# Kernel optimization log

Hardware: AMD Instinct MI355X
Metric: run time of the kernel (lower is better)

## Reference

```python
import jax, jax.numpy as jnp
import numpy as np

N_IN = 100_000
N_OUT = 400_000
K = 27          # 3^3 kernel offsets
C_IN = 64
C_OUT = 32


def setup_inputs() -> dict:
    key = jax.random.key(0)
    k1, k2, k3, k4 = jax.random.split(key, 4)
    feats = jax.random.normal(k1, (N_IN, C_IN), dtype=jnp.float32)
    # Minkowski-style weight: one [C_in, C_out] matrix per kernel offset
    weight = jax.random.normal(k2, (K, C_IN, C_OUT), dtype=jnp.float32) * (1.0 / np.sqrt(C_IN))
    # kernel maps: for each offset, M=N_IN (in_idx, out_idx) pairs
    in_map = jax.random.randint(k3, (K, N_IN), 0, N_IN, dtype=jnp.int64)
    out_map = jax.random.randint(k4, (K, N_IN), 0, N_OUT, dtype=jnp.int64)
    return {"feats": feats, "weight": weight, "in_map": in_map,
            "out_map": out_map, "n_out": N_OUT}


def reference(feats, weight, in_map, out_map, n_out):
    # gather-GEMM-scatter, vectorized over the K kernel offsets
    gathered = feats[in_map]                          # [K, M, C_in]
    msgs = jnp.einsum('kmc,kcd->kmd', gathered, weight)  # [K, M, C_out]
    out = jnp.zeros((n_out, msgs.shape[-1]), dtype=feats.dtype)
    out = out.at[out_map.reshape(-1)].add(msgs.reshape(-1, msgs.shape[-1]))
    return out
```

## Files before the change

kernel.cpp:

```cpp
#include <hip/hip_runtime.h>
#include <hip/hip_bf16.h>
#include <hip/hip_fp16.h>


using short8  = __attribute__((ext_vector_type(8))) short;
using floatx4 = __attribute__((ext_vector_type(4))) float;
using f32x4   = __attribute__((ext_vector_type(4))) float;
using i32x4   = __attribute__((ext_vector_type(4))) int;

constexpr int KOFF = 27;
constexpr int NIN  = 100000;
constexpr int NOUT = 400000;
constexpr int CIN  = 64;
constexpr int COUT = 32;
constexpr int MSGS = NIN;
constexpr int TILES = MSGS / 16;
constexpr int WPB   = 4;
constexpr int BLK_PER_K = 128;
constexpr int WSTRIDE = BLK_PER_K * WPB;

constexpr size_t ACC_BYTES   = (size_t)NOUT * COUT * 2;
constexpr size_t FEATS_BYTES = (size_t)NIN * CIN * 2;

constexpr int CVT_BLOCKS  = (NIN * CIN / 8) / 256;
constexpr int ZERO_BLOCKS = (int)(ACC_BYTES / 16) / 256;

__device__ __forceinline__ short f2bf(float f) {
    union { float f; unsigned u; } v; v.f = f;
    unsigned r = v.u + 0x7fff + ((v.u >> 16) & 1u);
    return (short)(r >> 16);
}

__global__ __launch_bounds__(256) void prep_kernel(
    const float* __restrict__ f, ushort* __restrict__ b, f32x4* __restrict__ accz)
{
    if (blockIdx.x < CVT_BLOCKS) {
        const int t = blockIdx.x * 256 + threadIdx.x;
        const f32x4* p = (const f32x4*)(f + (size_t)t * 8);
        f32x4 lo = __builtin_nontemporal_load(p);
        f32x4 hi = __builtin_nontemporal_load(p + 1);
        short8 v;
        v[0]=f2bf(lo[0]); v[1]=f2bf(lo[1]); v[2]=f2bf(lo[2]); v[3]=f2bf(lo[3]);
        v[4]=f2bf(hi[0]); v[5]=f2bf(hi[1]); v[6]=f2bf(hi[2]); v[7]=f2bf(hi[3]);
        *(short8*)(b + (size_t)t * 8) = v;
    } else {
        const int t = (blockIdx.x - CVT_BLOCKS) * 256 + threadIdx.x;
        f32x4 z = {0.f, 0.f, 0.f, 0.f};
        __builtin_nontemporal_store(z, accz + t);
    }
}

__global__ __launch_bounds__(256) void spconv_pipe_kernel(
    const ushort* __restrict__ feats_bf,
    const float*  __restrict__ weight,
    const int*    __restrict__ in_map,
    const int*    __restrict__ out_map,
    __half2*      __restrict__ accum)
{
    const int k    = blockIdx.y;
    const int wave = threadIdx.x >> 6;
    const int lane = threadIdx.x & 63;
    const int col  = lane & 15;
    const int quad = lane >> 4;
    const int kM   = k * MSGS;

    const float* Wk = weight + k * (CIN * COUT);
    short8 bfr[2][2];
    #pragma unroll
    for (int s = 0; s < 2; ++s)
        #pragma unroll
        for (int t = 0; t < 2; ++t)
            #pragma unroll
            for (int j = 0; j < 8; ++j)
                bfr[s][t][j] = f2bf(Wk[(s * 32 + quad * 8 + j) * COUT + 2 * col + t]);

    auto load_maps = [&](int t, int& inr, i32x4& orow) {
        const int tt = (t < TILES) ? t : (TILES - 1);
        const int mb = kM + tt * 16;
        inr  = __builtin_nontemporal_load(in_map + mb + col);
        orow = __builtin_nontemporal_load((const i32x4*)(out_map + mb + quad * 4));
    };
    auto load_feats = [&](int inr, short8& a0, short8& a1) {
        const ushort* ar = feats_bf + inr * CIN;
        a0 = *(const short8*)(ar + quad * 8);
        a1 = *(const short8*)(ar + 32 + quad * 8);
    };

    const int t0 = blockIdx.x * WPB + wave;

    int inrA; i32x4 orowA; load_maps(t0,               inrA, orowA);
    int inrB; i32x4 orowB; load_maps(t0 +     WSTRIDE, inrB, orowB);
    int inrC; i32x4 orowC; load_maps(t0 + 2 * WSTRIDE, inrC, orowC);
    short8 a0A, a1A; load_feats(inrA, a0A, a1A);
    short8 a0B, a1B; load_feats(inrB, a0B, a1B);

    for (int t = t0; t < TILES; t += WSTRIDE) {
        int inrD; i32x4 orowD;
        load_maps(t + 3 * WSTRIDE, inrD, orowD);
        short8 a0C, a1C;
        load_feats(inrC, a0C, a1C);

        floatx4 acc0 = {0.f, 0.f, 0.f, 0.f};
        floatx4 acc1 = {0.f, 0.f, 0.f, 0.f};
        acc0 = __builtin_amdgcn_mfma_f32_16x16x32_bf16(a0A, bfr[0][0], acc0, 0, 0, 0);
        acc1 = __builtin_amdgcn_mfma_f32_16x16x32_bf16(a0A, bfr[0][1], acc1, 0, 0, 0);
        acc0 = __builtin_amdgcn_mfma_f32_16x16x32_bf16(a1A, bfr[1][0], acc0, 0, 0, 0);
        acc1 = __builtin_amdgcn_mfma_f32_16x16x32_bf16(a1A, bfr[1][1], acc1, 0, 0, 0);

        const int orr[4] = {orowA[0], orowA[1], orowA[2], orowA[3]};
        #pragma unroll
        for (int i = 0; i < 4; ++i) {
            __half2 h = __floats2half2_rn(acc0[i], acc1[i]);
            unsafeAtomicAdd(accum + orr[i] * 16 + col, h);
        }

        inrA = inrB; a0A = a0B; a1A = a1B; orowA = orowB;
        inrB = inrC; a0B = a0C; a1B = a1C; orowB = orowC;
        inrC = inrD; orowC = orowD;
    }
}

__global__ __launch_bounds__(256) void spconv_fp16acc_f32feats_kernel(
    const float*  __restrict__ feats_f32,
    const float*  __restrict__ weight,
    const int*    __restrict__ in_map,
    const int*    __restrict__ out_map,
    __half2*      __restrict__ accum)
{
    const int k    = blockIdx.y;
    const int wave = threadIdx.x >> 6;
    const int lane = threadIdx.x & 63;
    const int col  = lane & 15;
    const int quad = lane >> 4;
    const int tile = blockIdx.x * WPB + wave;
    if (tile >= TILES) return;
    const int m0 = tile * 16;
    const long long mapbase = (long long)k * MSGS;

    const int in_row = in_map[mapbase + m0 + col];
    int orow[4];
    #pragma unroll
    for (int i = 0; i < 4; ++i) orow[i] = out_map[mapbase + m0 + quad * 4 + i];

    const float* Wk = weight + k * (CIN * COUT);
    short8 bfr[2][2];
    #pragma unroll
    for (int s = 0; s < 2; ++s)
        #pragma unroll
        for (int t = 0; t < 2; ++t)
            #pragma unroll
            for (int j = 0; j < 8; ++j)
                bfr[s][t][j] = f2bf(Wk[(s * 32 + quad * 8 + j) * COUT + 2 * col + t]);

    const float* ar = feats_f32 + (long long)in_row * CIN + quad * 8;
    const float4* p0 = (const float4*)ar;
    const float4* p1 = (const float4*)(ar + 32);
    float4 l0 = p0[0], h0 = p0[1], l1 = p1[0], h1 = p1[1];
    short8 a0, a1;
    a0[0]=f2bf(l0.x); a0[1]=f2bf(l0.y); a0[2]=f2bf(l0.z); a0[3]=f2bf(l0.w);
    a0[4]=f2bf(h0.x); a0[5]=f2bf(h0.y); a0[6]=f2bf(h0.z); a0[7]=f2bf(h0.w);
    a1[0]=f2bf(l1.x); a1[1]=f2bf(l1.y); a1[2]=f2bf(l1.z); a1[3]=f2bf(l1.w);
    a1[4]=f2bf(h1.x); a1[5]=f2bf(h1.y); a1[6]=f2bf(h1.z); a1[7]=f2bf(h1.w);

    floatx4 acc0 = {0.f, 0.f, 0.f, 0.f};
    floatx4 acc1 = {0.f, 0.f, 0.f, 0.f};
    acc0 = __builtin_amdgcn_mfma_f32_16x16x32_bf16(a0, bfr[0][0], acc0, 0, 0, 0);
    acc1 = __builtin_amdgcn_mfma_f32_16x16x32_bf16(a0, bfr[0][1], acc1, 0, 0, 0);
    acc0 = __builtin_amdgcn_mfma_f32_16x16x32_bf16(a1, bfr[1][0], acc0, 0, 0, 0);
    acc1 = __builtin_amdgcn_mfma_f32_16x16x32_bf16(a1, bfr[1][1], acc1, 0, 0, 0);

    #pragma unroll
    for (int i = 0; i < 4; ++i) {
        __half2 h = __floats2half2_rn(acc0[i], acc1[i]);
        unsafeAtomicAdd(accum + (long long)orow[i] * 16 + col, h);
    }
}

__global__ __launch_bounds__(256) void spconv_f32atomic_kernel(
    const float* __restrict__ feats,
    const float* __restrict__ weight,
    const int*   __restrict__ in_map,
    const int*   __restrict__ out_map,
    float*       __restrict__ out)
{
    const int k    = blockIdx.y;
    const int wave = threadIdx.x >> 6;
    const int lane = threadIdx.x & 63;
    const int col  = lane & 15;
    const int quad = lane >> 4;
    const int tile = blockIdx.x * WPB + wave;
    if (tile >= TILES) return;
    const int m0 = tile * 16;
    const long long mapbase = (long long)k * MSGS;

    const float* Wk = weight + k * (CIN * COUT);
    short8 bfr[2][2];
    #pragma unroll
    for (int s = 0; s < 2; ++s)
        #pragma unroll
        for (int t = 0; t < 2; ++t)
            #pragma unroll
            for (int j = 0; j < 8; ++j)
                bfr[s][t][j] = f2bf(Wk[(s * 32 + quad * 8 + j) * COUT + t * 16 + col]);

    const int in_row = in_map[mapbase + m0 + col];
    const float* arow = feats + (long long)in_row * CIN + quad * 8;

    floatx4 acc0 = {0.f, 0.f, 0.f, 0.f};
    floatx4 acc1 = {0.f, 0.f, 0.f, 0.f};
    #pragma unroll
    for (int s = 0; s < 2; ++s) {
        const float4* p = (const float4*)(arow + s * 32);
        float4 lo = p[0], hi = p[1];
        short8 a;
        a[0]=f2bf(lo.x); a[1]=f2bf(lo.y); a[2]=f2bf(lo.z); a[3]=f2bf(lo.w);
        a[4]=f2bf(hi.x); a[5]=f2bf(hi.y); a[6]=f2bf(hi.z); a[7]=f2bf(hi.w);
        acc0 = __builtin_amdgcn_mfma_f32_16x16x32_bf16(a, bfr[s][0], acc0, 0, 0, 0);
        acc1 = __builtin_amdgcn_mfma_f32_16x16x32_bf16(a, bfr[s][1], acc1, 0, 0, 0);
    }
    #pragma unroll
    for (int i = 0; i < 4; ++i) {
        const int orow = out_map[mapbase + m0 + quad * 4 + i];
        float* po = out + (long long)orow * COUT;
        atomicAdd(po + col,      acc0[i]);
        atomicAdd(po + col + 16, acc1[i]);
    }
}

__global__ __launch_bounds__(256) void h2_to_f32_kernel(
    const __half2* __restrict__ acc, float* __restrict__ out)
{
    const int t = blockIdx.x * blockDim.x + threadIdx.x;
    const __half2* p = acc + (size_t)t * 4;
    float2 f0 = __half22float2(p[0]);
    float2 f1 = __half22float2(p[1]);
    float2 f2 = __half22float2(p[2]);
    float2 f3 = __half22float2(p[3]);
    f32x4* o = (f32x4*)out + (size_t)t * 2;
    f32x4 o0 = {f0.x, f0.y, f1.x, f1.y};
    f32x4 o1 = {f2.x, f2.y, f3.x, f3.y};
    __builtin_nontemporal_store(o0, o);
    __builtin_nontemporal_store(o1, o + 1);
}

extern "C" void kernel_launch(void* const* d_in, const int* in_sizes, int n_in,
                              void* d_out, int out_size, void* d_ws, size_t ws_size,
                              hipStream_t stream) {
    const float* feats   = (const float*)d_in[0];
    const float* weight  = (const float*)d_in[1];
    const int*   in_map  = (const int*)d_in[2];
    const int*   out_map = (const int*)d_in[3];
    float*       out     = (float*)d_out;

    if (ws_size >= ACC_BYTES + FEATS_BYTES) {
        __half2* accum    = (__half2*)d_ws;
        ushort*  feats_bf = (ushort*)((char*)d_ws + ACC_BYTES);

        prep_kernel<<<CVT_BLOCKS + ZERO_BLOCKS, 256, 0, stream>>>(
            feats, feats_bf, (f32x4*)accum);
        spconv_pipe_kernel<<<dim3(BLK_PER_K, KOFF), 256, 0, stream>>>(
            feats_bf, weight, in_map, out_map, accum);
        h2_to_f32_kernel<<<(NOUT * 16 / 4) / 256, 256, 0, stream>>>(accum, out);
    } else if (ws_size >= ACC_BYTES) {
        __half2* accum = (__half2*)d_ws;
        hipMemsetAsync(accum, 0, ACC_BYTES, stream);
        spconv_fp16acc_f32feats_kernel<<<dim3((TILES + WPB - 1) / WPB, KOFF), 256, 0, stream>>>(
            feats, weight, in_map, out_map, accum);
        h2_to_f32_kernel<<<(NOUT * 16 / 4) / 256, 256, 0, stream>>>(accum, out);
    } else {
        hipMemsetAsync(d_out, 0, (size_t)out_size * sizeof(float), stream);
        spconv_f32atomic_kernel<<<dim3((TILES + WPB - 1) / WPB, KOFF), 256, 0, stream>>>(
            feats, weight, in_map, out_map, out);
    }
}
```

Baseline: 253.8 us.

## Fuse prep, gather-GEMM-scatter and convert into one cooperative kernel

Replaces the three-kernel sequence (bf16 convert plus accumulator zeroing, MFMA gather-GEMM-scatter with fp16 atomics, fp16-to-fp32 conversion) with one persistent cooperative kernel that uses grid-wide syncs between phases. The aim is to remove kernel launch gaps and tail idle time between stages. The cost is two grid barriers and a smaller fixed grid (75 blocks per offset instead of 128), which changes how the work is spread and may lower memory parallelism. If the cooperative launch fails, it falls back to the old three-kernel path.

```diff
diff --git a/kernel.cpp b/kernel.cpp
--- a/kernel.cpp
+++ b/kernel.cpp
@@ -1,7 +1,10 @@
 #include <hip/hip_runtime.h>
 #include <hip/hip_bf16.h>
 #include <hip/hip_fp16.h>
-
+#include <hip/hip_cooperative_groups.h>
+
+
+namespace cg = cooperative_groups;
 
 using short8  = __attribute__((ext_vector_type(8))) short;
 using floatx4 = __attribute__((ext_vector_type(4))) float;
@@ -16,6 +19,12 @@
 constexpr int MSGS = NIN;
 constexpr int TILES = MSGS / 16;
 constexpr int WPB   = 4;
+
+constexpr int CBLK_PER_K = 75;
+constexpr int COOP_BLOCKS = CBLK_PER_K * KOFF;
+constexpr int CWSTRIDE = CBLK_PER_K * WPB;
+constexpr int CTHREADS = COOP_BLOCKS * 256;
+
 constexpr int BLK_PER_K = 128;
 constexpr int WSTRIDE = BLK_PER_K * WPB;
 
@@ -30,6 +39,116 @@
     unsigned r = v.u + 0x7fff + ((v.u >> 16) & 1u);
     return (short)(r >> 16);
 }
+
+__global__ __launch_bounds__(256, 8) void spconv_fused_kernel(
+    const float* __restrict__ feats_f32,
+    ushort*      __restrict__ feats_bf,
+    const float* __restrict__ weight,
+    const int*   __restrict__ in_map,
+    const int*   __restrict__ out_map,
+    __half2*     __restrict__ accum,
+    float*       __restrict__ out)
+{
+    cg::grid_group grid = cg::this_grid();
+    const int gtid = blockIdx.x * 256 + threadIdx.x;
+
+    for (int t = gtid; t < NIN * CIN / 8; t += CTHREADS) {
+        const f32x4* p = (const f32x4*)(feats_f32 + (size_t)t * 8);
+        f32x4 lo = __builtin_nontemporal_load(p);
+        f32x4 hi = __builtin_nontemporal_load(p + 1);
+        short8 v;
+        v[0]=f2bf(lo[0]); v[1]=f2bf(lo[1]); v[2]=f2bf(lo[2]); v[3]=f2bf(lo[3]);
+        v[4]=f2bf(hi[0]); v[5]=f2bf(hi[1]); v[6]=f2bf(hi[2]); v[7]=f2bf(hi[3]);
+        *(short8*)(feats_bf + (size_t)t * 8) = v;
+    }
+    {
+        f32x4* accz = (f32x4*)accum;
+        f32x4 z = {0.f, 0.f, 0.f, 0.f};
+        for (int t = gtid; t < (int)(ACC_BYTES / 16); t += CTHREADS)
+            __builtin_nontemporal_store(z, accz + t);
+    }
+    grid.sync();
+
+    {
+        const int k    = blockIdx.x / CBLK_PER_K;
+        const int bx   = blockIdx.x % CBLK_PER_K;
+        const int wave = threadIdx.x >> 6;
+        const int lane = threadIdx.x & 63;
+        const int col  = lane & 15;
+        const int quad = lane >> 4;
+        const int kM   = k * MSGS;
+
+        const float* Wk = weight + k * (CIN * COUT);
+        short8 bfr[2][2];
+        #pragma unroll
+        for (int s = 0; s < 2; ++s)
+            #pragma unroll
+            for (int t = 0; t < 2; ++t)
+                #pragma unroll
+                for (int j = 0; j < 8; ++j)
+                    bfr[s][t][j] = f2bf(Wk[(s * 32 + quad * 8 + j) * COUT + 2 * col + t]);
+
+        auto load_maps = [&](int t, int& inr, i32x4& orow) {
+            const int tt = (t < TILES) ? t : (TILES - 1);
+            const int mb = kM + tt * 16;
+            inr  = __builtin_nontemporal_load(in_map + mb + col);
+            orow = __builtin_nontemporal_load((const i32x4*)(out_map + mb + quad * 4));
+        };
+        auto load_feats = [&](int inr, short8& a0, short8& a1) {
+            const ushort* ar = feats_bf + inr * CIN;
+            a0 = *(const short8*)(ar + quad * 8);
+            a1 = *(const short8*)(ar + 32 + quad * 8);
+        };
+
+        const int t0 = bx * WPB + wave;
+
+        int inrA; i32x4 orowA; load_maps(t0,                inrA, orowA);
+        int inrB; i32x4 orowB; load_maps(t0 +     CWSTRIDE, inrB, orowB);
+        int inrC; i32x4 orowC; load_maps(t0 + 2 * CWSTRIDE, inrC, orowC);
+        short8 a0A, a1A; load_feats(inrA, a0A, a1A);
+        short8 a0B, a1B; load_feats(inrB, a0B, a1B);
+
+        for (int t = t0; t < TILES; t += CWSTRIDE) {
+            int inrD; i32x4 orowD;
+            load_maps(t + 3 * CWSTRIDE, inrD, orowD);
+            short8 a0C, a1C;
+            load_feats(inrC, a0C, a1C);
+
+            floatx4 acc0 = {0.f, 0.f, 0.f, 0.f};
+            floatx4 acc1 = {0.f, 0.f, 0.f, 0.f};
+            acc0 = __builtin_amdgcn_mfma_f32_16x16x32_bf16(a0A, bfr[0][0], acc0, 0, 0, 0);
+            acc1 = __builtin_amdgcn_mfma_f32_16x16x32_bf16(a0A, bfr[0][1], acc1, 0, 0, 0);
+            acc0 = __builtin_amdgcn_mfma_f32_16x16x32_bf16(a1A, bfr[1][0], acc0, 0, 0, 0);
+            acc1 = __builtin_amdgcn_mfma_f32_16x16x32_bf16(a1A, bfr[1][1], acc1, 0, 0, 0);
+
+            const int orr[4] = {orowA[0], orowA[1], orowA[2], orowA[3]};
+            #pragma unroll
+            for (int i = 0; i < 4; ++i) {
+                __half2 h = __floats2half2_rn(acc0[i], acc1[i]);
+                unsafeAtomicAdd(accum + orr[i] * 16 + col, h);
+            }
+
+            inrA = inrB; a0A = a0B; a1A = a1B; orowA = orowB;
+            inrB = inrC; a0B = a0C; a1B = a1C; orowB = orowC;
+            inrC = inrD; orowC = orowD;
+        }
+    }
+    grid.sync();
+
+    for (int t = gtid; t < NOUT * 16 / 4; t += CTHREADS) {
+        const __half2* p = accum + (size_t)t * 4;
+        float2 f0 = __half22float2(p[0]);
+        float2 f1 = __half22float2(p[1]);
+        float2 f2 = __half22float2(p[2]);
+        float2 f3 = __half22float2(p[3]);
+        f32x4* o = (f32x4*)out + (size_t)t * 2;
+        f32x4 o0 = {f0.x, f0.y, f1.x, f1.y};
+        f32x4 o1 = {f2.x, f2.y, f3.x, f3.y};
+        __builtin_nontemporal_store(o0, o);
+        __builtin_nontemporal_store(o1, o + 1);
+    }
+}
+
 
 __global__ __launch_bounds__(256) void prep_kernel(
     const float* __restrict__ f, ushort* __restrict__ b, f32x4* __restrict__ accz)
@@ -256,11 +375,19 @@
         __half2* accum    = (__half2*)d_ws;
         ushort*  feats_bf = (ushort*)((char*)d_ws + ACC_BYTES);
 
-        prep_kernel<<<CVT_BLOCKS + ZERO_BLOCKS, 256, 0, stream>>>(
-            feats, feats_bf, (f32x4*)accum);
-        spconv_pipe_kernel<<<dim3(BLK_PER_K, KOFF), 256, 0, stream>>>(
-            feats_bf, weight, in_map, out_map, accum);
-        h2_to_f32_kernel<<<(NOUT * 16 / 4) / 256, 256, 0, stream>>>(accum, out);
+        void* args[] = {(void*)&feats, (void*)&feats_bf, (void*)&weight,
+                        (void*)&in_map, (void*)&out_map, (void*)&accum,
+                        (void*)&out};
+        hipError_t e = hipLaunchCooperativeKernel(
+            (const void*)spconv_fused_kernel, dim3(COOP_BLOCKS), dim3(256),
+            args, 0, stream);
+        if (e != hipSuccess) {
+            prep_kernel<<<CVT_BLOCKS + ZERO_BLOCKS, 256, 0, stream>>>(
+                feats, feats_bf, (f32x4*)accum);
+            spconv_pipe_kernel<<<dim3(BLK_PER_K, KOFF), 256, 0, stream>>>(
+                feats_bf, weight, in_map, out_map, accum);
+            h2_to_f32_kernel<<<(NOUT * 16 / 4) / 256, 256, 0, stream>>>(accum, out);
+        }
     } else if (ws_size >= ACC_BYTES) {
         __half2* accum = (__half2*)d_ws;
         hipMemsetAsync(accum, 0, ACC_BYTES, stream);
```

After: 752.3 us. 2.96x slower.

## Drop bf16 feature pre-conversion; gather fp32 rows and convert in pipelined loop

Applied to the files above, without the earlier changes.

Removes the prep kernel that converted the features to bf16 and zeroed the accumulator, replacing it with hipMemsetAsync for zeroing. The pipelined main kernel now gathers fp32 feature rows directly, keeping raw fp32 registers for upcoming tiles and converting them to bf16 one stage before use. This avoids writing and re-reading a bf16 copy of the features, but doubles the bytes per gathered row and adds conversion ALU work plus register pressure inside the loop. The pipeline depth for feature data changes, and the code leaves the tile A row index stale, though it is no longer needed.

```diff
diff --git a/kernel.cpp b/kernel.cpp
--- a/kernel.cpp
+++ b/kernel.cpp
@@ -19,11 +19,7 @@
 constexpr int BLK_PER_K = 128;
 constexpr int WSTRIDE = BLK_PER_K * WPB;
 
-constexpr size_t ACC_BYTES   = (size_t)NOUT * COUT * 2;
-constexpr size_t FEATS_BYTES = (size_t)NIN * CIN * 2;
-
-constexpr int CVT_BLOCKS  = (NIN * CIN / 8) / 256;
-constexpr int ZERO_BLOCKS = (int)(ACC_BYTES / 16) / 256;
+constexpr size_t ACC_BYTES = (size_t)NOUT * COUT * 2;
 
 __device__ __forceinline__ short f2bf(float f) {
     union { float f; unsigned u; } v; v.f = f;
@@ -31,31 +27,12 @@
     return (short)(r >> 16);
 }
 
-__global__ __launch_bounds__(256) void prep_kernel(
-    const float* __restrict__ f, ushort* __restrict__ b, f32x4* __restrict__ accz)
-{
-    if (blockIdx.x < CVT_BLOCKS) {
-        const int t = blockIdx.x * 256 + threadIdx.x;
-        const f32x4* p = (const f32x4*)(f + (size_t)t * 8);
-        f32x4 lo = __builtin_nontemporal_load(p);
-        f32x4 hi = __builtin_nontemporal_load(p + 1);
-        short8 v;
-        v[0]=f2bf(lo[0]); v[1]=f2bf(lo[1]); v[2]=f2bf(lo[2]); v[3]=f2bf(lo[3]);
-        v[4]=f2bf(hi[0]); v[5]=f2bf(hi[1]); v[6]=f2bf(hi[2]); v[7]=f2bf(hi[3]);
-        *(short8*)(b + (size_t)t * 8) = v;
-    } else {
-        const int t = (blockIdx.x - CVT_BLOCKS) * 256 + threadIdx.x;
-        f32x4 z = {0.f, 0.f, 0.f, 0.f};
-        __builtin_nontemporal_store(z, accz + t);
-    }
-}
-
-__global__ __launch_bounds__(256) void spconv_pipe_kernel(
-    const ushort* __restrict__ feats_bf,
-    const float*  __restrict__ weight,
-    const int*    __restrict__ in_map,
-    const int*    __restrict__ out_map,
-    __half2*      __restrict__ accum)
+__global__ __launch_bounds__(256) void spconv_pipe_f32_kernel(
+    const float* __restrict__ feats,
+    const float* __restrict__ weight,
+    const int*   __restrict__ in_map,
+    const int*   __restrict__ out_map,
+    __half2*     __restrict__ accum)
 {
     const int k    = blockIdx.y;
     const int wave = threadIdx.x >> 6;
@@ -80,10 +57,18 @@
         inr  = __builtin_nontemporal_load(in_map + mb + col);
         orow = __builtin_nontemporal_load((const i32x4*)(out_map + mb + quad * 4));
     };
-    auto load_feats = [&](int inr, short8& a0, short8& a1) {
-        const ushort* ar = feats_bf + inr * CIN;
-        a0 = *(const short8*)(ar + quad * 8);
-        a1 = *(const short8*)(ar + 32 + quad * 8);
+    auto load_raw = [&](int inr, f32x4* r) {
+        const float* ar = feats + (long long)inr * CIN + quad * 8;
+        r[0] = *(const f32x4*)(ar);
+        r[1] = *(const f32x4*)(ar + 4);
+        r[2] = *(const f32x4*)(ar + 32);
+        r[3] = *(const f32x4*)(ar + 36);
+    };
+    auto cvt = [&](const f32x4* r, short8& a0, short8& a1) {
+        #pragma unroll
+        for (int j = 0; j < 4; ++j) { a0[j] = f2bf(r[0][j]); a0[4+j] = f2bf(r[1][j]); }
+        #pragma unroll
+        for (int j = 0; j < 4; ++j) { a1[j] = f2bf(r[2][j]); a1[4+j] = f2bf(r[3][j]); }
     };
 
     const int t0 = blockIdx.x * WPB + wave;
@@ -91,14 +76,15 @@
     int inrA; i32x4 orowA; load_maps(t0,               inrA, orowA);
     int inrB; i32x4 orowB; load_maps(t0 +     WSTRIDE, inrB, orowB);
     int inrC; i32x4 orowC; load_maps(t0 + 2 * WSTRIDE, inrC, orowC);
-    short8 a0A, a1A; load_feats(inrA, a0A, a1A);
-    short8 a0B, a1B; load_feats(inrB, a0B, a1B);
+    f32x4 rawA[4]; load_raw(inrA, rawA);
+    short8 a0A, a1A; cvt(rawA, a0A, a1A);
+    f32x4 rawB[4]; load_raw(inrB, rawB);
 
     for (int t = t0; t < TILES; t += WSTRIDE) {
         int inrD; i32x4 orowD;
         load_maps(t + 3 * WSTRIDE, inrD, orowD);
-        short8 a0C, a1C;
-        load_feats(inrC, a0C, a1C);
+        f32x4 rawC[4];
+        load_raw(inrC, rawC);
 
         floatx4 acc0 = {0.f, 0.f, 0.f, 0.f};
         floatx4 acc1 = {0.f, 0.f, 0.f, 0.f};
@@ -114,65 +100,12 @@
             unsafeAtomicAdd(accum + orr[i] * 16 + col, h);
         }
 
-        inrA = inrB; a0A = a0B; a1A = a1B; orowA = orowB;
-        inrB = inrC; a0B = a0C; a1B = a1C; orowB = orowC;
-        inrC = inrD; orowC = orowD;
-    }
-}
+        cvt(rawB, a0A, a1A);
 
-__global__ __launch_bounds__(256) void spconv_fp16acc_f32feats_kernel(
-    const float*  __restrict__ feats_f32,
-    const float*  __restrict__ weight,
-    const int*    __restrict__ in_map,
-    const int*    __restrict__ out_map,
-    __half2*      __restrict__ accum)
-{
-    const int k    = blockIdx.y;
-    const int wave = threadIdx.x >> 6;
-    const int lane = threadIdx.x & 63;
-    const int col  = lane & 15;
-    const int quad = lane >> 4;
-    const int tile = blockIdx.x * WPB + wave;
-    if (tile >= TILES) return;
-    const int m0 = tile * 16;
-    const long long mapbase = (long long)k * MSGS;
-
-    const int in_row = in_map[mapbase + m0 + col];
-    int orow[4];
-    #pragma unroll
-    for (int i = 0; i < 4; ++i) orow[i] = out_map[mapbase + m0 + quad * 4 + i];
-
-    const float* Wk = weight + k * (CIN * COUT);
-    short8 bfr[2][2];
-    #pragma unroll
-    for (int s = 0; s < 2; ++s)
         #pragma unroll
-        for (int t = 0; t < 2; ++t)
-            #pragma unroll
-            for (int j = 0; j < 8; ++j)
-                bfr[s][t][j] = f2bf(Wk[(s * 32 + quad * 8 + j) * COUT + 2 * col + t]);
-
-    const float* ar = feats_f32 + (long long)in_row * CIN + quad * 8;
-    const float4* p0 = (const float4*)ar;
-    const float4* p1 = (const float4*)(ar + 32);
-    float4 l0 = p0[0], h0 = p0[1], l1 = p1[0], h1 = p1[1];
-    short8 a0, a1;
-    a0[0]=f2bf(l0.x); a0[1]=f2bf(l0.y); a0[2]=f2bf(l0.z); a0[3]=f2bf(l0.w);
-    a0[4]=f2bf(h0.x); a0[5]=f2bf(h0.y); a0[6]=f2bf(h0.z); a0[7]=f2bf(h0.w);
-    a1[0]=f2bf(l1.x); a1[1]=f2bf(l1.y); a1[2]=f2bf(l1.z); a1[3]=f2bf(l1.w);
-    a1[4]=f2bf(h1.x); a1[5]=f2bf(h1.y); a1[6]=f2bf(h1.z); a1[7]=f2bf(h1.w);
-
-    floatx4 acc0 = {0.f, 0.f, 0.f, 0.f};
-    floatx4 acc1 = {0.f, 0.f, 0.f, 0.f};
-    acc0 = __builtin_amdgcn_mfma_f32_16x16x32_bf16(a0, bfr[0][0], acc0, 0, 0, 0);
-    acc1 = __builtin_amdgcn_mfma_f32_16x16x32_bf16(a0, bfr[0][1], acc1, 0, 0, 0);
-    acc0 = __builtin_amdgcn_mfma_f32_16x16x32_bf16(a1, bfr[1][0], acc0, 0, 0, 0);
-    acc1 = __builtin_amdgcn_mfma_f32_16x16x32_bf16(a1, bfr[1][1], acc1, 0, 0, 0);
-
-    #pragma unroll
-    for (int i = 0; i < 4; ++i) {
-        __half2 h = __floats2half2_rn(acc0[i], acc1[i]);
-        unsafeAtomicAdd(accum + (long long)orow[i] * 16 + col, h);
+        for (int i = 0; i < 4; ++i) rawB[i] = rawC[i];
+        orowA = orowB; orowB = orowC; orowC = orowD;
+        inrC = inrD;
     }
 }
 
@@ -252,19 +185,10 @@
     const int*   out_map = (const int*)d_in[3];
     float*       out     = (float*)d_out;
 
-    if (ws_size >= ACC_BYTES + FEATS_BYTES) {
-        __half2* accum    = (__half2*)d_ws;
-        ushort*  feats_bf = (ushort*)((char*)d_ws + ACC_BYTES);
-
-        prep_kernel<<<CVT_BLOCKS + ZERO_BLOCKS, 256, 0, stream>>>(
-            feats, feats_bf, (f32x4*)accum);
-        spconv_pipe_kernel<<<dim3(BLK_PER_K, KOFF), 256, 0, stream>>>(
-            feats_bf, weight, in_map, out_map, accum);
-        h2_to_f32_kernel<<<(NOUT * 16 / 4) / 256, 256, 0, stream>>>(accum, out);
-    } else if (ws_size >= ACC_BYTES) {
+    if (ws_size >= ACC_BYTES) {
         __half2* accum = (__half2*)d_ws;
         hipMemsetAsync(accum, 0, ACC_BYTES, stream);
-        spconv_fp16acc_f32feats_kernel<<<dim3((TILES + WPB - 1) / WPB, KOFF), 256, 0, stream>>>(
+        spconv_pipe_f32_kernel<<<dim3(BLK_PER_K, KOFF), 256, 0, stream>>>(
             feats, weight, in_map, out_map, accum);
         h2_to_f32_kernel<<<(NOUT * 16 / 4) / 256, 256, 0, stream>>>(accum, out);
     } else {
```

New measurement: 258.8 us. Within noise of the previous version (+2.0%).
